# Optimization experiments

Hardware: AMD Instinct MI355X
Metric: run time of the kernel (lower is better)

The kernel has to match this reference:

```python
import jax, jax.numpy as jnp
import numpy as np

EPS = float(np.finfo(np.float32).eps)
H = 256          # hidden_size
K = 10           # num_event_types
B, S = 32, 4096  # batch, seq_len


def _linear_params(kw, kb, fan_in, fan_out):
    # torch nn.Linear default init (uniform +-1/sqrt(fan_in)), then abs + clamp(min=eps)
    bound = 1.0 / np.sqrt(fan_in)
    w = jnp.clip(jnp.abs(jax.random.uniform(kw, (fan_out, fan_in), minval=-bound, maxval=bound, dtype=jnp.float32)), EPS)
    b = jnp.clip(jnp.abs(jax.random.uniform(kb, (fan_out,), minval=-bound, maxval=bound, dtype=jnp.float32)), EPS)
    return w, b


def setup_inputs() -> dict:
    key = jax.random.key(0)
    ks = jax.random.split(key, 12)
    w1, b1 = _linear_params(ks[0], ks[1], 1, H)        # layer_dense_1
    w2, b2 = _linear_params(ks[2], ks[3], 2 * H, H)    # layer_dense_2
    wA, bA = _linear_params(ks[4], ks[5], H, H)        # module_list[0]
    wB, bB = _linear_params(ks[6], ks[7], H, H)        # module_list[1]
    w3, b3 = _linear_params(ks[8], ks[9], H, K)        # layer_dense_3 linear
    hidden_states = jax.random.normal(ks[10], (B, S, H), dtype=jnp.float32)
    time_delta_seqs = jax.random.uniform(ks[11], (B, S), dtype=jnp.float32)
    return dict(hidden_states=hidden_states, time_delta_seqs=time_delta_seqs,
                w1=w1, b1=b1, w2=w2, b2=b2, wA=wA, bA=bA, wB=wB, bB=bB, w3=w3, b3=b3)


def _cumul_hazard(td, h, w1, b1, w2, b2, wA, bA, wB, bB, w3, b3):
    # layer_dense_1: Linear(1 -> H) on td[..., None]
    t = td[..., None] * w1[:, 0] + b1                      # [B,S,H]
    out = jnp.tanh(jnp.concatenate([h, t], axis=-1) @ w2.T + b2)  # [B,S,H]
    out = jnp.tanh(out @ wA.T + bA)
    out = jnp.tanh(out @ wB.T + bB)
    return jax.nn.softplus(out @ w3.T + b3)                # [B,S,K]


def reference(hidden_states, time_delta_seqs, w1, b1, w2, b2, wA, bA, wB, bB, w3, b3):
    f = lambda td: _cumul_hazard(td, hidden_states, w1, b1, w2, b2, wA, bA, wB, bB, w3, b3)
    # Each output element depends only on its own t[b,s] (elementwise in time),
    # so a single forward-mode JVP with tangent=ones yields the exact per-element
    # derivative for ALL event types at once (fuses torch's per-type grad loop).
    integral_lambda, d_dt = jax.jvp(f, (time_delta_seqs,), (jnp.ones_like(time_delta_seqs),))
    # torch takes grad of .mean() over [B,S], which scales the derivative by 1/(B*S)
    derivative_integral_lambda = d_dt / time_delta_seqs.size
    return integral_lambda, derivative_integral_lambda
```

## Files before the change

### kernel.cpp

```cpp
#include <hip/hip_runtime.h>
#include <hip/hip_bf16.h>
#include <stdint.h>

typedef __bf16 bf16x8 __attribute__((ext_vector_type(8)));
typedef __bf16 bf16x4 __attribute__((ext_vector_type(4)));
typedef float  f32x4  __attribute__((ext_vector_type(4)));
typedef float  f32x2  __attribute__((ext_vector_type(2)));

#define MFMA16(a,b,c) __builtin_amdgcn_mfma_f32_16x16x32_bf16((a),(b),(c),0,0,0)

static constexpr int H_   = 256;
static constexpr int KEV  = 10;
static constexpr int NTOK = 32 * 4096;
static constexpr int NCHUNK = 48;

__device__ __forceinline__ float ptanh(float x){
    float t = x * x;
    float n = fmaf(t, t + 105.0f, 945.0f);
    float d = fmaf(t, fmaf(t, 15.0f, 420.0f), 945.0f);
    float r = x * n * __builtin_amdgcn_rcpf(d);
    return fminf(1.0f, fmaxf(-1.0f, r));
}

__device__ __forceinline__ void cp16(void* lds, const void* g){
    auto l = reinterpret_cast<__attribute__((address_space(3))) uint32_t*>(
                 (uint32_t)reinterpret_cast<uintptr_t>(lds));
    auto s = reinterpret_cast<const __attribute__((address_space(1))) uint32_t*>(
                 reinterpret_cast<uintptr_t>(g));
    __builtin_amdgcn_global_load_lds(s, l, 16, 0, 0);
}

__device__ __forceinline__ bf16x8 cvtFrag(const float* p){
    f32x4 a = *(const f32x4*)p;
    f32x4 b = *(const f32x4*)(p + 4);
    bf16x8 r;
    #pragma unroll
    for (int j = 0; j < 4; ++j){ r[j] = (__bf16)a[j]; r[4 + j] = (__bf16)b[j]; }
    return r;
}

__global__ void prep_vc(const float* __restrict__ w1, const float* __restrict__ b1,
                        const float* __restrict__ w2, const float* __restrict__ b2,
                        float* __restrict__ vc){
    int j = blockIdx.x * 4 + (threadIdx.x >> 6);
    int l = threadIdx.x & 63;
    const float* row = w2 + (size_t)j * (2 * H_) + H_;
    float v = 0.f, cc = 0.f;
    #pragma unroll
    for (int i = 0; i < 4; ++i){
        int k = l + 64 * i;
        float w = row[k];
        v  += w * w1[k];
        cc += w * b1[k];
    }
    #pragma unroll
    for (int off = 32; off; off >>= 1){
        v  += __shfl_down(v,  off, 64);
        cc += __shfl_down(cc, off, 64);
    }
    if (l == 0){ vc[j] = v; vc[H_ + j] = cc + b2[j]; }
}

__global__ void prep_pack(const float* __restrict__ w2, const float* __restrict__ wA,
                          const float* __restrict__ wB, __hip_bfloat16* __restrict__ pk){
    int b  = blockIdx.x;
    int L  = b >> 4, n0 = b & 15;
    const float* W = (L == 0) ? w2 : ((L == 1) ? wA : wB);
    int K = (L == 0) ? 2 * H_ : H_;
    __hip_bfloat16* dst = pk + (size_t)b * 4096;
    int t = threadIdx.x;
    #pragma unroll
    for (int u = 0; u < 2; ++u){
        int slot = t * 2 + u;
        int s = slot >> 6, q = (slot >> 4) & 3, c = slot & 15;
        const float* src = W + (size_t)(n0 * 16 + c) * K + 32 * s + 8 * q;
        #pragma unroll
        for (int j = 0; j < 8; ++j) dst[slot * 8 + j] = __float2bfloat16(src[j]);
    }
}

__global__ __launch_bounds__(256, 2) void chfn_kernel(
    const float* __restrict__ hs, const float* __restrict__ td,
    const __hip_bfloat16* __restrict__ wpk,
    const float* __restrict__ bA, const float* __restrict__ bB,
    const float* __restrict__ w3, const float* __restrict__ b3,
    const float* __restrict__ vc,
    float* __restrict__ out)
{
    __shared__ __hip_bfloat16 sA[4 * 16 * H_];
    __shared__ __hip_bfloat16 sD[4 * 16 * H_];
    __shared__ __hip_bfloat16 wls[2][4096];

    const int tid  = threadIdx.x;
    const int wave = tid >> 6;
    const int lane = tid & 63;
    const int q    = lane >> 4;
    const int c    = lane & 15;
    const int tokenBase = blockIdx.x * 64 + wave * 16;
    const int wrow = wave * 16;

    const float* hrow = hs + (size_t)(tokenBase + c) * H_ + 8 * q;
    f32x4 h0[8], h1[8];
    #pragma unroll
    for (int s = 0; s < 8; ++s){
        h0[s] = *(const f32x4*)(hrow + 32 * s);
        h1[s] = *(const f32x4*)(hrow + 32 * s + 4);
    }

    #pragma unroll
    for (int j = 0; j < 2; ++j){
        int i = wave * 2 + j;
        cp16((char*)&wls[0][0] + i * 1024, (const char*)wpk + i * 1024 + lane * 16);
    }

    float myTd = td[tokenBase + c];

    bf16x8 aF[8], aB[8];
    #pragma unroll
    for (int s = 0; s < 8; ++s){
        bf16x8 rr;
        #pragma unroll
        for (int j = 0; j < 4; ++j){ rr[j] = (__bf16)h0[s][j]; rr[4 + j] = (__bf16)h1[s][j]; }
        aF[s] = rr;
    }

    __syncthreads();

    int g = 0;
    #pragma unroll 1
    for (int n0 = 0; n0 < 16; ++n0, ++g){
        const __hip_bfloat16* cur = wls[g & 1];
        {
            const char* src = (const char*)(wpk + (size_t)(g + 1) * 4096);
            #pragma unroll
            for (int j = 0; j < 2; ++j){
                int i = wave * 2 + j;
                cp16((char*)&wls[(g + 1) & 1][0] + i * 1024, src + i * 1024 + lane * 16);
            }
        }
        f32x4 fa = {0.f,0.f,0.f,0.f}, fb = {0.f,0.f,0.f,0.f};
        #pragma unroll
        for (int s = 0; s < 4; ++s){
            bf16x8 bv0 = *(const bf16x8*)(cur + ((s * 4 + q) * 16 + c) * 8);
            bf16x8 bv1 = *(const bf16x8*)(cur + (((s + 4) * 4 + q) * 16 + c) * 8);
            fa = MFMA16(bv0, aF[s],     fa);
            fb = MFMA16(bv1, aF[s + 4], fb);
        }
        int nb = n0 * 16 + 4 * q;
        f32x4 v4 = *(const f32x4*)(vc + nb);
        f32x4 c4 = *(const f32x4*)(vc + H_ + nb);
        bf16x4 pa, pd;
        #pragma unroll
        for (int r = 0; r < 4; ++r){
            float x  = (fa[r] + fb[r]) + fmaf(myTd, v4[r], c4[r]);
            float th = ptanh(x);
            float dd = fmaf(-th, th, 1.0f) * v4[r];
            pa[r] = (__bf16)th; pd[r] = (__bf16)dd;
        }
        int ch  = 2 * n0 + (q >> 1);
        int off = (wrow + c) * H_ + (((ch + c) & 31) << 3) + ((q & 1) << 2);
        *(bf16x4*)((void*)(sA + off)) = pa;
        *(bf16x4*)((void*)(sD + off)) = pd;
        __syncthreads();
    }

    const float* bias2[2] = {bA, bB};
    #pragma unroll 1
    for (int L = 0; L < 2; ++L){
        const float* bias = bias2[L];
        const __hip_bfloat16* arow = sA + (wrow + c) * H_;
        const __hip_bfloat16* drow = sD + (wrow + c) * H_;
        #pragma unroll
        for (int s = 0; s < 8; ++s){
            int chn = (((4 * s + q) + c) & 31) << 3;
            aF[s] = *(const bf16x8*)(arow + chn);
            aB[s] = *(const bf16x8*)(drow + chn);
        }
        #pragma unroll 1
        for (int n0 = 0; n0 < 16; ++n0, ++g){
            const __hip_bfloat16* cur = wls[g & 1];
            if (g + 1 < NCHUNK){
                const char* src = (const char*)(wpk + (size_t)(g + 1) * 4096);
                #pragma unroll
                for (int j = 0; j < 2; ++j){
                    int i = wave * 2 + j;
                    cp16((char*)&wls[(g + 1) & 1][0] + i * 1024, src + i * 1024 + lane * 16);
                }
            }
            f32x4 fa = {0.f,0.f,0.f,0.f}, fb = {0.f,0.f,0.f,0.f};
            f32x4 ga = {0.f,0.f,0.f,0.f}, gb = {0.f,0.f,0.f,0.f};
            #pragma unroll
            for (int s = 0; s < 4; ++s){
                bf16x8 bv0 = *(const bf16x8*)(cur + ((s * 4 + q) * 16 + c) * 8);
                bf16x8 bv1 = *(const bf16x8*)(cur + (((s + 4) * 4 + q) * 16 + c) * 8);
                fa = MFMA16(bv0, aF[s],     fa);
                ga = MFMA16(bv0, aB[s],     ga);
                fb = MFMA16(bv1, aF[s + 4], fb);
                gb = MFMA16(bv1, aB[s + 4], gb);
            }
            int nb = n0 * 16 + 4 * q;
            f32x4 b4 = *(const f32x4*)(bias + nb);
            bf16x4 pa, pd;
            #pragma unroll
            for (int r = 0; r < 4; ++r){
                float th = ptanh((fa[r] + fb[r]) + b4[r]);
                float dd = fmaf(-th, th, 1.0f) * (ga[r] + gb[r]);
                pa[r] = (__bf16)th; pd[r] = (__bf16)dd;
            }
            int ch  = 2 * n0 + (q >> 1);
            int off = (wrow + c) * H_ + (((ch + c) & 31) << 3) + ((q & 1) << 2);
            *(bf16x4*)((void*)(sA + off)) = pa;
            *(bf16x4*)((void*)(sD + off)) = pd;
            __syncthreads();
        }
    }

    {
        const __hip_bfloat16* arow = sA + (wrow + c) * H_;
        const __hip_bfloat16* drow = sD + (wrow + c) * H_;
        #pragma unroll
        for (int s = 0; s < 8; ++s){
            int chn = (((4 * s + q) + c) & 31) << 3;
            aF[s] = *(const bf16x8*)(arow + chn);
            aB[s] = *(const bf16x8*)(drow + chn);
        }
        int crow = (c < KEV) ? c : 0;
        const float* wp0 = w3 + (size_t)crow * H_ + 8 * q;
        f32x4 fa = {0.f,0.f,0.f,0.f}, fb = {0.f,0.f,0.f,0.f};
        f32x4 ga = {0.f,0.f,0.f,0.f}, gb = {0.f,0.f,0.f,0.f};
        #pragma unroll
        for (int s = 0; s < 4; ++s){
            bf16x8 bv0 = cvtFrag(wp0 + 32 * s);
            bf16x8 bv1 = cvtFrag(wp0 + 32 * (s + 4));
            fa = MFMA16(bv0, aF[s],     fa);
            ga = MFMA16(bv0, aB[s],     ga);
            fb = MFMA16(bv1, aF[s + 4], fb);
            gb = MFMA16(bv1, aB[s + 4], gb);
        }
        int fbase = 4 * q;
        size_t token = tokenBase + c;
        float sp[4], dv[4];
        #pragma unroll
        for (int r = 0; r < 4; ++r){
            int fi  = fbase + r;
            float bn = b3[(fi < KEV) ? fi : (KEV - 1)];
            float z  = (fa[r] + fb[r]) + bn;
            float a  = fabsf(z);
            float e  = __builtin_amdgcn_exp2f(-1.4426950408889634f * a);
            sp[r] = fmaxf(z, 0.f) + 0.69314718055994531f * __builtin_amdgcn_logf(1.0f + e);
            float sg = __builtin_amdgcn_rcpf(1.0f + e);
            sg = (z >= 0.f) ? sg : 1.0f - sg;
            dv[r] = sg * (ga[r] + gb[r]) * (1.0f / 131072.0f);
        }
        float* o0 = out + token * KEV + fbase;
        float* o1 = out + (size_t)NTOK * KEV + token * KEV + fbase;
        if (q < 2){
            *(f32x2*)o0       = (f32x2){sp[0], sp[1]};
            *(f32x2*)(o0 + 2) = (f32x2){sp[2], sp[3]};
            *(f32x2*)o1       = (f32x2){dv[0], dv[1]};
            *(f32x2*)(o1 + 2) = (f32x2){dv[2], dv[3]};
        } else if (q == 2){
            *(f32x2*)o0 = (f32x2){sp[0], sp[1]};
            *(f32x2*)o1 = (f32x2){dv[0], dv[1]};
        }
    }
}

extern "C" void kernel_launch(void* const* d_in, const int* in_sizes, int n_in,
                              void* d_out, int out_size, void* d_ws, size_t ws_size,
                              hipStream_t stream){
    const float* hs = (const float*)d_in[0];
    const float* td = (const float*)d_in[1];
    const float* w1 = (const float*)d_in[2];
    const float* b1 = (const float*)d_in[3];
    const float* w2 = (const float*)d_in[4];
    const float* b2 = (const float*)d_in[5];
    const float* wA = (const float*)d_in[6];
    const float* bA = (const float*)d_in[7];
    const float* wB = (const float*)d_in[8];
    const float* bB = (const float*)d_in[9];
    const float* w3 = (const float*)d_in[10];
    const float* b3 = (const float*)d_in[11];

    float*          vc  = (float*)d_ws;
    __hip_bfloat16* wpk = (__hip_bfloat16*)((char*)d_ws + 4096);
    float*          outp = (float*)d_out;

    prep_vc  <<<64, 256, 0, stream>>>(w1, b1, w2, b2, vc);
    prep_pack<<<48, 256, 0, stream>>>(w2, wA, wB, wpk);
    chfn_kernel<<<NTOK / 64, 256, 0, stream>>>(hs, td, wpk, bA, bB, w3, b3, vc, outp);
}
```

Measured before the change: 345.6 us.

## Load weight fragments directly into registers and process 32 tokens per wave

Weight chunks are now streamed straight from global memory into double-buffered registers instead of through an LDS double buffer filled by global_load_lds. Removing the shared weight buffer also removes every per-chunk __syncthreads, since each wave only touches its own rows of the activation scratch. Each wave now handles 32 tokens instead of 16, so every weight fragment feeds twice as many MFMAs. The cost is 128 KB of dynamic LDS per block with one block per CU, more register pressure, and repeated global/L2 weight reads from every wave.

```diff
diff --git a/kernel.cpp b/kernel.cpp
--- a/kernel.cpp
+++ b/kernel.cpp
@@ -12,7 +12,6 @@
 static constexpr int H_   = 256;
 static constexpr int KEV  = 10;
 static constexpr int NTOK = 32 * 4096;
-static constexpr int NCHUNK = 48;
 
 __device__ __forceinline__ float ptanh(float x){
     float t = x * x;
@@ -20,14 +19,6 @@
     float d = fmaf(t, fmaf(t, 15.0f, 420.0f), 945.0f);
     float r = x * n * __builtin_amdgcn_rcpf(d);
     return fminf(1.0f, fmaxf(-1.0f, r));
-}
-
-__device__ __forceinline__ void cp16(void* lds, const void* g){
-    auto l = reinterpret_cast<__attribute__((address_space(3))) uint32_t*>(
-                 (uint32_t)reinterpret_cast<uintptr_t>(lds));
-    auto s = reinterpret_cast<const __attribute__((address_space(1))) uint32_t*>(
-                 reinterpret_cast<uintptr_t>(g));
-    __builtin_amdgcn_global_load_lds(s, l, 16, 0, 0);
 }
 
 __device__ __forceinline__ bf16x8 cvtFrag(const float* p){
@@ -79,7 +70,7 @@
     }
 }
 
-__global__ __launch_bounds__(256, 2) void chfn_kernel(
+__global__ __launch_bounds__(256, 1) void chfn_kernel(
     const float* __restrict__ hs, const float* __restrict__ td,
     const __hip_bfloat16* __restrict__ wpk,
     const float* __restrict__ bA, const float* __restrict__ bB,
@@ -87,181 +78,208 @@
     const float* __restrict__ vc,
     float* __restrict__ out)
 {
-    __shared__ __hip_bfloat16 sA[4 * 16 * H_];
-    __shared__ __hip_bfloat16 sD[4 * 16 * H_];
-    __shared__ __hip_bfloat16 wls[2][4096];
+    extern __shared__ __hip_bfloat16 smem[];
+    __hip_bfloat16* sA = smem;
+    __hip_bfloat16* sD = smem + 128 * H_;
 
     const int tid  = threadIdx.x;
     const int wave = tid >> 6;
     const int lane = tid & 63;
     const int q    = lane >> 4;
     const int c    = lane & 15;
-    const int tokenBase = blockIdx.x * 64 + wave * 16;
-    const int wrow = wave * 16;
-
-    const float* hrow = hs + (size_t)(tokenBase + c) * H_ + 8 * q;
-    f32x4 h0[8], h1[8];
-    #pragma unroll
-    for (int s = 0; s < 8; ++s){
-        h0[s] = *(const f32x4*)(hrow + 32 * s);
-        h1[s] = *(const f32x4*)(hrow + 32 * s + 4);
-    }
-
-    #pragma unroll
-    for (int j = 0; j < 2; ++j){
-        int i = wave * 2 + j;
-        cp16((char*)&wls[0][0] + i * 1024, (const char*)wpk + i * 1024 + lane * 16);
-    }
-
-    float myTd = td[tokenBase + c];
-
-    bf16x8 aF[8], aB[8];
-    #pragma unroll
-    for (int s = 0; s < 8; ++s){
-        bf16x8 rr;
-        #pragma unroll
-        for (int j = 0; j < 4; ++j){ rr[j] = (__bf16)h0[s][j]; rr[4 + j] = (__bf16)h1[s][j]; }
-        aF[s] = rr;
-    }
-
-    __syncthreads();
-
-    int g = 0;
-    #pragma unroll 1
-    for (int n0 = 0; n0 < 16; ++n0, ++g){
-        const __hip_bfloat16* cur = wls[g & 1];
+    const int tb   = blockIdx.x * 128 + wave * 32;
+    const int baseRow = wave * 32;
+
+    const bf16x8* wp = (const bf16x8*)wpk;
+    const int ws = q * 16 + c;
+
+    bf16x8 W0[8], W1[8];
+    {
+        const bf16x8* b = wp + ws;
+        #pragma unroll
+        for (int s = 0; s < 8; ++s) W0[s] = b[s * 64];
+    }
+
+    bf16x8 aF0[8], aF1[8], aB0[8], aB1[8];
+    {
+        const float* h0 = hs + (size_t)(tb + c) * H_ + 8 * q;
+        const float* h1 = hs + (size_t)(tb + 16 + c) * H_ + 8 * q;
+        #pragma unroll
+        for (int s = 0; s < 8; ++s){
+            aF0[s] = cvtFrag(h0 + 32 * s);
+            aF1[s] = cvtFrag(h1 + 32 * s);
+        }
+    }
+    float td0 = td[tb + c];
+    float td1 = td[tb + 16 + c];
+
+    #pragma unroll 2
+    for (int n0 = 0; n0 < 16; ++n0){
+        bf16x8* cur = (n0 & 1) ? W1 : W0;
+        bf16x8* nxt = (n0 & 1) ? W0 : W1;
         {
-            const char* src = (const char*)(wpk + (size_t)(g + 1) * 4096);
-            #pragma unroll
-            for (int j = 0; j < 2; ++j){
-                int i = wave * 2 + j;
-                cp16((char*)&wls[(g + 1) & 1][0] + i * 1024, src + i * 1024 + lane * 16);
-            }
-        }
-        f32x4 fa = {0.f,0.f,0.f,0.f}, fb = {0.f,0.f,0.f,0.f};
+            const bf16x8* b = wp + (size_t)(n0 + 1) * 512 + ws;
+            #pragma unroll
+            for (int s = 0; s < 8; ++s) nxt[s] = b[s * 64];
+        }
+        f32x4 v4 = *(const f32x4*)(vc + n0 * 16 + 4 * q);
+        f32x4 c4 = *(const f32x4*)(vc + H_ + n0 * 16 + 4 * q);
+        f32x4 fa0 = {0.f,0.f,0.f,0.f}, fb0 = {0.f,0.f,0.f,0.f};
+        f32x4 fa1 = {0.f,0.f,0.f,0.f}, fb1 = {0.f,0.f,0.f,0.f};
         #pragma unroll
         for (int s = 0; s < 4; ++s){
-            bf16x8 bv0 = *(const bf16x8*)(cur + ((s * 4 + q) * 16 + c) * 8);
-            bf16x8 bv1 = *(const bf16x8*)(cur + (((s + 4) * 4 + q) * 16 + c) * 8);
-            fa = MFMA16(bv0, aF[s],     fa);
-            fb = MFMA16(bv1, aF[s + 4], fb);
-        }
-        int nb = n0 * 16 + 4 * q;
-        f32x4 v4 = *(const f32x4*)(vc + nb);
-        f32x4 c4 = *(const f32x4*)(vc + H_ + nb);
-        bf16x4 pa, pd;
-        #pragma unroll
-        for (int r = 0; r < 4; ++r){
-            float x  = (fa[r] + fb[r]) + fmaf(myTd, v4[r], c4[r]);
-            float th = ptanh(x);
-            float dd = fmaf(-th, th, 1.0f) * v4[r];
-            pa[r] = (__bf16)th; pd[r] = (__bf16)dd;
-        }
-        int ch  = 2 * n0 + (q >> 1);
-        int off = (wrow + c) * H_ + (((ch + c) & 31) << 3) + ((q & 1) << 2);
-        *(bf16x4*)((void*)(sA + off)) = pa;
-        *(bf16x4*)((void*)(sD + off)) = pd;
-        __syncthreads();
-    }
-
-    const float* bias2[2] = {bA, bB};
+            fa0 = MFMA16(cur[s],     aF0[s],     fa0);
+            fa1 = MFMA16(cur[s],     aF1[s],     fa1);
+            fb0 = MFMA16(cur[s + 4], aF0[s + 4], fb0);
+            fb1 = MFMA16(cur[s + 4], aF1[s + 4], fb1);
+        }
+        #pragma unroll
+        for (int t = 0; t < 2; ++t){
+            const f32x4& fa = t ? fa1 : fa0;
+            const f32x4& fb = t ? fb1 : fb0;
+            float tdg = t ? td1 : td0;
+            bf16x4 pa, pd;
+            #pragma unroll
+            for (int r = 0; r < 4; ++r){
+                float x  = (fa[r] + fb[r]) + fmaf(tdg, v4[r], c4[r]);
+                float th = ptanh(x);
+                float dd = fmaf(-th, th, 1.0f) * v4[r];
+                pa[r] = (__bf16)th; pd[r] = (__bf16)dd;
+            }
+            int off = (baseRow + 16 * t + c) * H_ +
+                      (((2 * n0 + (q >> 1) + c) & 31) << 3) + ((q & 1) << 2);
+            *(bf16x4*)((void*)(sA + off)) = pa;
+            *(bf16x4*)((void*)(sD + off)) = pd;
+        }
+    }
+
     #pragma unroll 1
     for (int L = 0; L < 2; ++L){
-        const float* bias = bias2[L];
-        const __hip_bfloat16* arow = sA + (wrow + c) * H_;
-        const __hip_bfloat16* drow = sD + (wrow + c) * H_;
+        const float* bias = L ? bB : bA;
+        {
+            const __hip_bfloat16* a0 = sA + (baseRow + c) * H_;
+            const __hip_bfloat16* a1 = sA + (baseRow + 16 + c) * H_;
+            const __hip_bfloat16* d0 = sD + (baseRow + c) * H_;
+            const __hip_bfloat16* d1 = sD + (baseRow + 16 + c) * H_;
+            #pragma unroll
+            for (int s = 0; s < 8; ++s){
+                int chn = (((4 * s + q) + c) & 31) << 3;
+                aF0[s] = *(const bf16x8*)(a0 + chn);
+                aF1[s] = *(const bf16x8*)(a1 + chn);
+                aB0[s] = *(const bf16x8*)(d0 + chn);
+                aB1[s] = *(const bf16x8*)(d1 + chn);
+            }
+        }
+        #pragma unroll 2
+        for (int n0 = 0; n0 < 16; ++n0){
+            int g = 16 * (L + 1) + n0;
+            bf16x8* cur = (n0 & 1) ? W1 : W0;
+            bf16x8* nxt = (n0 & 1) ? W0 : W1;
+            {
+                int gn = g + 1; if (gn > 47) gn = 47;
+                const bf16x8* b = wp + (size_t)gn * 512 + ws;
+                #pragma unroll
+                for (int s = 0; s < 8; ++s) nxt[s] = b[s * 64];
+            }
+            f32x4 b4 = *(const f32x4*)(bias + n0 * 16 + 4 * q);
+            f32x4 fa0 = {0.f,0.f,0.f,0.f}, fb0 = {0.f,0.f,0.f,0.f};
+            f32x4 ga0 = {0.f,0.f,0.f,0.f}, gb0 = {0.f,0.f,0.f,0.f};
+            f32x4 fa1 = {0.f,0.f,0.f,0.f}, fb1 = {0.f,0.f,0.f,0.f};
+            f32x4 ga1 = {0.f,0.f,0.f,0.f}, gb1 = {0.f,0.f,0.f,0.f};
+            #pragma unroll
+            for (int s = 0; s < 4; ++s){
+                fa0 = MFMA16(cur[s],     aF0[s],     fa0);
+                ga0 = MFMA16(cur[s],     aB0[s],     ga0);
+                fa1 = MFMA16(cur[s],     aF1[s],     fa1);
+                ga1 = MFMA16(cur[s],     aB1[s],     ga1);
+                fb0 = MFMA16(cur[s + 4], aF0[s + 4], fb0);
+                gb0 = MFMA16(cur[s + 4], aB0[s + 4], gb0);
+                fb1 = MFMA16(cur[s + 4], aF1[s + 4], fb1);
+                gb1 = MFMA16(cur[s + 4], aB1[s + 4], gb1);
+            }
+            #pragma unroll
+            for (int t = 0; t < 2; ++t){
+                const f32x4& fa = t ? fa1 : fa0;  const f32x4& fb = t ? fb1 : fb0;
+                const f32x4& ga = t ? ga1 : ga0;  const f32x4& gb = t ? gb1 : gb0;
+                bf16x4 pa, pd;
+                #pragma unroll
+                for (int r = 0; r < 4; ++r){
+                    float th = ptanh((fa[r] + fb[r]) + b4[r]);
+                    float dd = fmaf(-th, th, 1.0f) * (ga[r] + gb[r]);
+                    pa[r] = (__bf16)th; pd[r] = (__bf16)dd;
+                }
+                int off = (baseRow + 16 * t + c) * H_ +
+                          (((2 * n0 + (q >> 1) + c) & 31) << 3) + ((q & 1) << 2);
+                *(bf16x4*)((void*)(sA + off)) = pa;
+                *(bf16x4*)((void*)(sD + off)) = pd;
+            }
+        }
+    }
+
+    {
+        const __hip_bfloat16* a0 = sA + (baseRow + c) * H_;
+        const __hip_bfloat16* a1 = sA + (baseRow + 16 + c) * H_;
+        const __hip_bfloat16* d0 = sD + (baseRow + c) * H_;
+        const __hip_bfloat16* d1 = sD + (baseRow + 16 + c) * H_;
         #pragma unroll
         for (int s = 0; s < 8; ++s){
             int chn = (((4 * s + q) + c) & 31) << 3;
-            aF[s] = *(const bf16x8*)(arow + chn);
-            aB[s] = *(const bf16x8*)(drow + chn);
-        }
-        #pragma unroll 1
-        for (int n0 = 0; n0 < 16; ++n0, ++g){
-            const __hip_bfloat16* cur = wls[g & 1];
-            if (g + 1 < NCHUNK){
-                const char* src = (const char*)(wpk + (size_t)(g + 1) * 4096);
-                #pragma unroll
-                for (int j = 0; j < 2; ++j){
-                    int i = wave * 2 + j;
-                    cp16((char*)&wls[(g + 1) & 1][0] + i * 1024, src + i * 1024 + lane * 16);
-                }
-            }
-            f32x4 fa = {0.f,0.f,0.f,0.f}, fb = {0.f,0.f,0.f,0.f};
-            f32x4 ga = {0.f,0.f,0.f,0.f}, gb = {0.f,0.f,0.f,0.f};
-            #pragma unroll
-            for (int s = 0; s < 4; ++s){
-                bf16x8 bv0 = *(const bf16x8*)(cur + ((s * 4 + q) * 16 + c) * 8);
-                bf16x8 bv1 = *(const bf16x8*)(cur + (((s + 4) * 4 + q) * 16 + c) * 8);
-                fa = MFMA16(bv0, aF[s],     fa);
-                ga = MFMA16(bv0, aB[s],     ga);
-                fb = MFMA16(bv1, aF[s + 4], fb);
-                gb = MFMA16(bv1, aB[s + 4], gb);
-            }
-            int nb = n0 * 16 + 4 * q;
-            f32x4 b4 = *(const f32x4*)(bias + nb);
-            bf16x4 pa, pd;
+            aF0[s] = *(const bf16x8*)(a0 + chn);
+            aF1[s] = *(const bf16x8*)(a1 + chn);
+            aB0[s] = *(const bf16x8*)(d0 + chn);
+            aB1[s] = *(const bf16x8*)(d1 + chn);
+        }
+        int crow = (c < KEV) ? c : 0;
+        const float* wp3 = w3 + (size_t)crow * H_ + 8 * q;
+        bf16x8 w3f[8];
+        #pragma unroll
+        for (int s = 0; s < 8; ++s) w3f[s] = cvtFrag(wp3 + 32 * s);
+
+        f32x4 fa0 = {0.f,0.f,0.f,0.f}, fb0 = {0.f,0.f,0.f,0.f};
+        f32x4 ga0 = {0.f,0.f,0.f,0.f}, gb0 = {0.f,0.f,0.f,0.f};
+        f32x4 fa1 = {0.f,0.f,0.f,0.f}, fb1 = {0.f,0.f,0.f,0.f};
+        f32x4 ga1 = {0.f,0.f,0.f,0.f}, gb1 = {0.f,0.f,0.f,0.f};
+        #pragma unroll
+        for (int s = 0; s < 4; ++s){
+            fa0 = MFMA16(w3f[s],     aF0[s],     fa0);
+            ga0 = MFMA16(w3f[s],     aB0[s],     ga0);
+            fa1 = MFMA16(w3f[s],     aF1[s],     fa1);
+            ga1 = MFMA16(w3f[s],     aB1[s],     ga1);
+            fb0 = MFMA16(w3f[s + 4], aF0[s + 4], fb0);
+            gb0 = MFMA16(w3f[s + 4], aB0[s + 4], gb0);
+            fb1 = MFMA16(w3f[s + 4], aF1[s + 4], fb1);
+            gb1 = MFMA16(w3f[s + 4], aB1[s + 4], gb1);
+        }
+        int fbase = 4 * q;
+        #pragma unroll
+        for (int t = 0; t < 2; ++t){
+            const f32x4& fa = t ? fa1 : fa0;  const f32x4& fb = t ? fb1 : fb0;
+            const f32x4& ga = t ? ga1 : ga0;  const f32x4& gb = t ? gb1 : gb0;
+            size_t token = tb + 16 * t + c;
+            float sp[4], dv[4];
             #pragma unroll
             for (int r = 0; r < 4; ++r){
-                float th = ptanh((fa[r] + fb[r]) + b4[r]);
-                float dd = fmaf(-th, th, 1.0f) * (ga[r] + gb[r]);
-                pa[r] = (__bf16)th; pd[r] = (__bf16)dd;
-            }
-            int ch  = 2 * n0 + (q >> 1);
-            int off = (wrow + c) * H_ + (((ch + c) & 31) << 3) + ((q & 1) << 2);
-            *(bf16x4*)((void*)(sA + off)) = pa;
-            *(bf16x4*)((void*)(sD + off)) = pd;
-            __syncthreads();
-        }
-    }
-
-    {
-        const __hip_bfloat16* arow = sA + (wrow + c) * H_;
-        const __hip_bfloat16* drow = sD + (wrow + c) * H_;
-        #pragma unroll
-        for (int s = 0; s < 8; ++s){
-            int chn = (((4 * s + q) + c) & 31) << 3;
-            aF[s] = *(const bf16x8*)(arow + chn);
-            aB[s] = *(const bf16x8*)(drow + chn);
-        }
-        int crow = (c < KEV) ? c : 0;
-        const float* wp0 = w3 + (size_t)crow * H_ + 8 * q;
-        f32x4 fa = {0.f,0.f,0.f,0.f}, fb = {0.f,0.f,0.f,0.f};
-        f32x4 ga = {0.f,0.f,0.f,0.f}, gb = {0.f,0.f,0.f,0.f};
-        #pragma unroll
-        for (int s = 0; s < 4; ++s){
-            bf16x8 bv0 = cvtFrag(wp0 + 32 * s);
-            bf16x8 bv1 = cvtFrag(wp0 + 32 * (s + 4));
-            fa = MFMA16(bv0, aF[s],     fa);
-            ga = MFMA16(bv0, aB[s],     ga);
-            fb = MFMA16(bv1, aF[s + 4], fb);
-            gb = MFMA16(bv1, aB[s + 4], gb);
-        }
-        int fbase = 4 * q;
-        size_t token = tokenBase + c;
-        float sp[4], dv[4];
-        #pragma unroll
-        for (int r = 0; r < 4; ++r){
-            int fi  = fbase + r;
-            float bn = b3[(fi < KEV) ? fi : (KEV - 1)];
-            float z  = (fa[r] + fb[r]) + bn;
-            float a  = fabsf(z);
-            float e  = __builtin_amdgcn_exp2f(-1.4426950408889634f * a);
-            sp[r] = fmaxf(z, 0.f) + 0.69314718055994531f * __builtin_amdgcn_logf(1.0f + e);
-            float sg = __builtin_amdgcn_rcpf(1.0f + e);
-            sg = (z >= 0.f) ? sg : 1.0f - sg;
-            dv[r] = sg * (ga[r] + gb[r]) * (1.0f / 131072.0f);
-        }
-        float* o0 = out + token * KEV + fbase;
-        float* o1 = out + (size_t)NTOK * KEV + token * KEV + fbase;
-        if (q < 2){
-            *(f32x2*)o0       = (f32x2){sp[0], sp[1]};
-            *(f32x2*)(o0 + 2) = (f32x2){sp[2], sp[3]};
-            *(f32x2*)o1       = (f32x2){dv[0], dv[1]};
-            *(f32x2*)(o1 + 2) = (f32x2){dv[2], dv[3]};
-        } else if (q == 2){
-            *(f32x2*)o0 = (f32x2){sp[0], sp[1]};
-            *(f32x2*)o1 = (f32x2){dv[0], dv[1]};
+                int fi   = fbase + r;
+                float bn = b3[(fi < KEV) ? fi : (KEV - 1)];
+                float z  = (fa[r] + fb[r]) + bn;
+                float a  = fabsf(z);
+                float e  = __builtin_amdgcn_exp2f(-1.4426950408889634f * a);
+                sp[r] = fmaxf(z, 0.f) + 0.69314718055994531f * __builtin_amdgcn_logf(1.0f + e);
+                float sg = __builtin_amdgcn_rcpf(1.0f + e);
+                sg = (z >= 0.f) ? sg : 1.0f - sg;
+                dv[r] = sg * (ga[r] + gb[r]) * (1.0f / 131072.0f);
+            }
+            float* o0 = out + token * KEV + fbase;
+            float* o1 = out + (size_t)NTOK * KEV + token * KEV + fbase;
+            if (q < 2){
+                *(f32x2*)o0       = (f32x2){sp[0], sp[1]};
+                *(f32x2*)(o0 + 2) = (f32x2){sp[2], sp[3]};
+                *(f32x2*)o1       = (f32x2){dv[0], dv[1]};
+                *(f32x2*)(o1 + 2) = (f32x2){dv[2], dv[3]};
+            } else if (q == 2){
+                *(f32x2*)o0 = (f32x2){sp[0], sp[1]};
+                *(f32x2*)o1 = (f32x2){dv[0], dv[1]};
+            }
         }
     }
 }
@@ -286,7 +304,10 @@
     __hip_bfloat16* wpk = (__hip_bfloat16*)((char*)d_ws + 4096);
     float*          outp = (float*)d_out;
 
+    (void)hipFuncSetAttribute((const void*)chfn_kernel,
+                              hipFuncAttributeMaxDynamicSharedMemorySize, 131072);
+
     prep_vc  <<<64, 256, 0, stream>>>(w1, b1, w2, b2, vc);
     prep_pack<<<48, 256, 0, stream>>>(w2, wA, wB, wpk);
-    chfn_kernel<<<NTOK / 64, 256, 0, stream>>>(hs, td, wpk, bA, bB, w3, b3, vc, outp);
-}
+    chfn_kernel<<<NTOK / 128, 256, 131072, stream>>>(hs, td, wpk, bA, bB, w3, b3, vc, outp);
+}
```

Result: slower. 353.2 us (+2.2%).
